# Performance work log

Measured on AMD Instinct MI355X. Metric: run time of the kernel, lower is better.

## Reference

```python
import jax, jax.numpy as jnp
import numpy as np

N_QUBITS = 8
N_LAYERS = 4
DIM = 2 ** N_QUBITS  # 256 state-vector

# PauliZ sign table: signs[i, idx] = +1 if bit of wire i in basis index idx is 0 else -1.
# Wire 0 is the most-significant axis (state axes ordered wire0..wire{n-1}).
_idx = np.arange(DIM)
SIGNS = np.stack([1.0 - 2.0 * ((_idx >> (N_QUBITS - 1 - i)) & 1) for i in range(N_QUBITS)]).astype(np.float32)  # [n, 256]


def _rx_mat(theta):
    c = jnp.cos(0.5 * theta).astype(jnp.complex64)
    s = (-1j * jnp.sin(0.5 * theta)).astype(jnp.complex64)
    return jnp.stack([jnp.stack([c, s]), jnp.stack([s, c])])  # [2,2]


def _rz_diag(theta):
    return jnp.stack([jnp.exp(-0.5j * theta), jnp.exp(0.5j * theta)]).astype(jnp.complex64)  # [2]


def _apply_1q(state, U, w):
    # state: (2,)*n complex64; apply 2x2 U on wire w
    st = jnp.moveaxis(state, w, 0).reshape(2, -1)
    st = U @ st
    return jnp.moveaxis(st.reshape((2,) * N_QUBITS), 0, w)


def _apply_diag(state, d, w):
    st = jnp.moveaxis(state, w, 0)
    st = st * d.reshape((2,) + (1,) * (N_QUBITS - 1))
    return jnp.moveaxis(st, 0, w)


def _cnot(state, c, t):
    st = jnp.moveaxis(state, (c, t), (0, 1))
    st = jnp.stack([st[0], st[1][::-1]], axis=0)  # flip target where control==1
    return jnp.moveaxis(st, (0, 1), (c, t))


def _circuit(angles, weights):
    # angles: [n_qubits], weights: [n_layers, 2, n_qubits] -> expvals [n_qubits]
    state = jnp.zeros((2,) * N_QUBITS, jnp.complex64).at[(0,) * N_QUBITS].set(1.0)
    for i in range(N_QUBITS):
        state = _apply_1q(state, _rx_mat(angles[i]), i)
        state = _apply_diag(state, _rz_diag(angles[i]), i)
    for l in range(N_LAYERS):
        for i in range(N_QUBITS):
            state = _apply_1q(state, _rx_mat(weights[l, 0, i]), i)
            state = _apply_diag(state, _rz_diag(weights[l, 1, i]), i)
        for i in range(N_QUBITS - 1):
            state = _cnot(state, i, i + 1)
    probs = jnp.abs(state.reshape(-1)) ** 2  # [256]
    return (probs @ SIGNS.T).astype(jnp.float32)  # [n_qubits] <Z_i>


def setup_inputs() -> dict:
    key = jax.random.key(0)
    B, D_IN, D_OUT = 8192, 1024, 1024
    ks = jax.random.split(key, 6)
    bound_in = np.sqrt(6.0 / D_IN)  # kaiming_uniform fan_in, linear
    bound_out = np.sqrt(6.0 / N_QUBITS)
    return {
        "x": jax.random.normal(ks[0], (B, D_IN), jnp.float32),
        "W_in": jax.random.uniform(ks[1], (N_QUBITS, D_IN), jnp.float32, -bound_in, bound_in),
        "b_in": jnp.zeros((N_QUBITS,), jnp.float32),
        "q_weights": jax.random.uniform(ks[2], (N_LAYERS, 2, N_QUBITS), jnp.float32, 0.0, 2.0 * np.pi),
        "W_out": jax.random.uniform(ks[3], (D_OUT, N_QUBITS), jnp.float32, -bound_out, bound_out),
        "b_out": jnp.zeros((D_OUT,), jnp.float32),
    }


def reference(x, W_in, b_in, q_weights, W_out, b_out):
    x_proj = x @ W_in.T + b_in                                   # [B, n_qubits]
    ev = jax.vmap(_circuit, in_axes=(0, None))(x_proj, q_weights)  # [B, n_qubits]
    return ev @ W_out.T + b_out                                   # [B, output_dim]
```

## Files before the change

### kernel.cpp

```cpp
#include <hip/hip_runtime.h>
#include <math.h>


typedef float f32x2 __attribute__((ext_vector_type(2)));

__device__ __forceinline__ int f2i(float v) { return __float_as_int(v); }
__device__ __forceinline__ float i2f(int v) { return __int_as_float(v); }

template <int CTRL>
__device__ __forceinline__ float dppf(float v) {
    return i2f(__builtin_amdgcn_update_dpp(0, f2i(v), CTRL, 0xF, 0xF, true));
}

template <int ML>
__device__ __forceinline__ float gshm(float v) {
    static_assert(ML > 0 && ML < 64, "lane mask");
    if constexpr (ML == 1)      return dppf<0xB1>(v);
    else if constexpr (ML == 2) return dppf<0x4E>(v);
    else if constexpr (ML == 3) return dppf<0x1B>(v);
    else if constexpr (ML == 8) return dppf<0x128>(v);
    else if constexpr (ML < 32) return i2f(__builtin_amdgcn_ds_swizzle(f2i(v), 0x1F | (ML << 10)));
    else                        return __shfl_xor(v, ML, 64);
}

template <int L>
__device__ __forceinline__ float rdlane(float v) {
    return i2f(__builtin_amdgcn_readlane(f2i(v), L));
}

template <int ML, int MR, int ZL, int ZR>
__device__ __forceinline__ void ggate(f32x2& reA, f32x2& reB, f32x2& imA, f32x2& imB,
                                      float c1, float s1, float c2, float s2,
                                      int lane) {
    f32x2 sReA, sReB, sImA, sImB;
    if constexpr (MR == 0)      { sReA = reA;    sReB = reB;    sImA = imA;    sImB = imB; }
    else if constexpr (MR == 1) { sReA = reA.yx; sReB = reB.yx; sImA = imA.yx; sImB = imB.yx; }
    else if constexpr (MR == 2) { sReA = reB;    sReB = reA;    sImA = imB;    sImB = imA; }
    else                        { sReA = reB.yx; sReB = reA.yx; sImA = imB.yx; sImB = imA.yx; }
    f32x2 pReA, pReB, pImA, pImB;
    if constexpr (ML != 0) {
        pReA.x = gshm<ML>(sReA.x); pReA.y = gshm<ML>(sReA.y);
        pReB.x = gshm<ML>(sReB.x); pReB.y = gshm<ML>(sReB.y);
        pImA.x = gshm<ML>(sImA.x); pImA.y = gshm<ML>(sImA.y);
        pImB.x = gshm<ML>(sImB.x); pImB.y = gshm<ML>(sImB.y);
    } else { pReA = sReA; pReB = sReB; pImA = sImA; pImB = sImB; }
    f32x2 nReA = c1 * reA + s1 * pImA;
    f32x2 nReB = c1 * reB + s1 * pImB;
    f32x2 nImA = c1 * imA - s1 * pReA;
    f32x2 nImB = c1 * imB - s1 * pReB;
    float base;
    if constexpr (ZL == 0) base = -s2;
    else                   base = (__popc(lane & ZL) & 1) ? s2 : -s2;
    constexpr bool N1 = (ZR & 1) != 0;
    constexpr bool N2 = ((ZR >> 1) & 1) != 0;
    constexpr bool N3 = (((ZR & 1) ^ ((ZR >> 1) & 1)) != 0);
    f32x2 ssA = { base, N1 ? -base : base };
    f32x2 ssB = { N2 ? -base : base, N3 ? -base : base };
    f32x2 tA = c2 * nReA - ssA * nImA;
    f32x2 tB = c2 * nReB - ssB * nImB;
    imA = c2 * nImA + ssA * nReA;
    imB = c2 * nImB + ssB * nReB;
    reA = tA;
    reB = tB;
}

__global__ void __launch_bounds__(256, 8) qasa_kernel(
    const float* __restrict__ x, const float* __restrict__ W_in,
    const float* __restrict__ b_in, const float* __restrict__ qw,
    const float* __restrict__ W_out, const float* __restrict__ b_out,
    float* __restrict__ out)
{
    const int tid = threadIdx.x;
    const int lane = tid & 63;
    const int w = tid >> 6;
    const int block4 = blockIdx.x * 4;

    __shared__ float ang[32];
    __shared__ float evs[4][8] __attribute__((aligned(16)));

    float vc, vs;
    __sincosf(0.5f * qw[lane], &vs, &vc);

    const int b0 = lane & 1, b1 = (lane >> 1) & 1, b3 = (lane >> 3) & 1;
    const int qofl = b0 | (b1 << 1) | (b3 << 2);
    const float binq = b_in[qofl];

    {
        const float4* w4 = (const float4*)W_in;
        const float4* xr0 = (const float4*)(x + (size_t)block4 * 1024);
        f32x2 acc2[8];
#pragma unroll
        for (int j = 0; j < 8; ++j) acc2[j] = (f32x2){0.f, 0.f};
#pragma unroll
        for (int k = 0; k < 4; ++k) {
            float4 wv0 = w4[(2 * w) * 256 + lane + 64 * k];
            float4 wv1 = w4[(2 * w + 1) * 256 + lane + 64 * k];
#pragma unroll
            for (int r = 0; r < 4; ++r) {
                float4 xvv = xr0[r * 256 + lane + 64 * k];
                acc2[r]     += (f32x2){xvv.x, xvv.y} * (f32x2){wv0.x, wv0.y}
                             + (f32x2){xvv.z, xvv.w} * (f32x2){wv0.z, wv0.w};
                acc2[4 + r] += (f32x2){xvv.x, xvv.y} * (f32x2){wv1.x, wv1.y}
                             + (f32x2){xvv.z, xvv.w} * (f32x2){wv1.z, wv1.w};
            }
        }
        float acc[8];
#pragma unroll
        for (int j = 0; j < 8; ++j) {
            acc[j] = acc2[j].x + acc2[j].y;
            acc[j] += dppf<0xB1>(acc[j]);
            acc[j] += dppf<0x4E>(acc[j]);
            acc[j] += dppf<0x128>(acc[j]);
        }
        float t01 = b0 ? acc[1] : acc[0];
        float t23 = b0 ? acc[3] : acc[2];
        float t45 = b0 ? acc[5] : acc[4];
        float t67 = b0 ? acc[7] : acc[6];
        float ta = b1 ? t23 : t01;
        float tb = b1 ? t67 : t45;
        float S = b3 ? tb : ta;
        S += gshm<4>(S); S += gshm<16>(S); S += gshm<32>(S);
        if ((lane & 52) == 0)
            ang[(2 * w + ((lane >> 3) & 1)) * 4 + (lane & 3)] = S;
    }
    __syncthreads();

    float A = ang[qofl * 4 + w] + binq;
    float ca, sa;
    __sincosf(0.5f * A, &sa, &ca);
    float ur = ca * ca, ui = -ca * sa, vr = sa * sa, vi = ui;
    const int a1 = 4 * qofl, a2 = 4 * (qofl + 8);
    float cx = i2f(__builtin_amdgcn_ds_bpermute(a1, f2i(vc)));
    float sx = i2f(__builtin_amdgcn_ds_bpermute(a1, f2i(vs)));
    float cz = i2f(__builtin_amdgcn_ds_bpermute(a2, f2i(vc)));
    float sz = i2f(__builtin_amdgcn_ds_bpermute(a2, f2i(vs)));
    float ur1 = cx * ur + sx * vi, ui1 = cx * ui - sx * vr;
    float vr1 = cx * vr + sx * ui, vi1 = cx * vi - sx * ur;
    float ur2 = cz * ur1 + sz * ui1, ui2 = cz * ui1 - sz * ur1;
    float vr2 = cz * vr1 - sz * vi1, vi2 = cz * vi1 + sz * vr1;

    float Pr, Pi;
    {
        float fur = rdlane<0>(ur2), fui = rdlane<0>(ui2);
        float fvr = rdlane<0>(vr2), fvi = rdlane<0>(vi2);
        bool b = (lane >> 5) & 1;
        Pr = b ? fvr : fur;
        Pi = b ? fvi : fui;
    }
#define PMUL(W_, L_) { \
        float fur = rdlane<L_>(ur2), fui = rdlane<L_>(ui2); \
        float fvr = rdlane<L_>(vr2), fvi = rdlane<L_>(vi2); \
        bool b = (lane >> (5 - (W_))) & 1; \
        float fr = b ? fvr : fur, fi = b ? fvi : fui; \
        float tr = Pr * fr - Pi * fi; \
        Pi = Pr * fi + Pi * fr; \
        Pr = tr; }
    PMUL(1, 1) PMUL(2, 2) PMUL(3, 3) PMUL(4, 8) PMUL(5, 9)
#undef PMUL
    f32x2 reA, reB, imA, imB;
    {
        float u6r = rdlane<10>(ur2), u6i = rdlane<10>(ui2);
        float v6r = rdlane<10>(vr2), v6i = rdlane<10>(vi2);
        float u7r = rdlane<11>(ur2), u7i = rdlane<11>(ui2);
        float v7r = rdlane<11>(vr2), v7i = rdlane<11>(vi2);
        float rr[4], ii[4];
#pragma unroll
        for (int r = 0; r < 4; ++r) {
            float g6r_ = (r & 2) ? v6r : u6r, g6i_ = (r & 2) ? v6i : u6i;
            float g7r_ = (r & 1) ? v7r : u7r, g7i_ = (r & 1) ? v7i : u7i;
            float fr = g6r_ * g7r_ - g6i_ * g7i_;
            float fi = g6r_ * g7i_ + g6i_ * g7r_;
            rr[r] = Pr * fr - Pi * fi;
            ii[r] = Pr * fi + Pi * fr;
        }
        reA = (f32x2){ rr[0], rr[1] };  reB = (f32x2){ rr[2], rr[3] };
        imA = (f32x2){ ii[0], ii[1] };  imB = (f32x2){ ii[2], ii[3] };
    }

#define GG(Lx, W_, ML_, MR_, ZL_, ZR_) \
    ggate<ML_, MR_, ZL_, ZR_>(reA, reB, imA, imB, \
        rdlane<16 * (Lx) + (W_)>(vc), rdlane<16 * (Lx) + (W_)>(vs), \
        rdlane<16 * (Lx) + 8 + (W_)>(vc), rdlane<16 * (Lx) + 8 + (W_)>(vs), lane);

    GG(1,0, 48,0, 32,0)  GG(1,1, 24,0, 48,0)  GG(1,2, 12,0, 56,0) GG(1,3, 6,0, 60,0)
    GG(1,4, 3,0, 62,0)   GG(1,5, 1,2, 63,0)   GG(1,6, 0,3, 63,2)  GG(1,7, 0,1, 63,3)
    GG(2,0, 40,0, 32,0)  GG(2,1, 20,0, 16,0)  GG(2,2, 10,0, 40,0) GG(2,3, 5,0, 20,0)
    GG(2,4, 2,2, 42,0)   GG(2,5, 1,1, 21,0)   GG(2,6, 0,2, 42,2)  GG(2,7, 0,1, 21,1)
    GG(3,0, 60,0, 32,0)  GG(3,1, 30,0, 48,0)  GG(3,2, 15,0, 24,0) GG(3,3, 7,2, 12,0)
    GG(3,4, 3,3, 38,0)   GG(3,5, 1,3, 51,0)   GG(3,6, 0,3, 25,2)  GG(3,7, 0,1, 12,3)
#undef GG

    {
        float p0 = reA.x * reA.x + imA.x * imA.x;
        float p1 = reA.y * reA.y + imA.y * imA.y;
        float p2 = reB.x * reB.x + imB.x * imB.x;
        float p3 = reB.y * reB.y + imB.y * imB.y;
        float q0 = (p0 + p1) + (p2 + p3);
        float q2 = (p0 + p1) - (p2 + p3);
        float q1 = (p0 + p2) - (p1 + p3);

        float v = q0;
        { float u = dppf<0xB1>(v);  v = (lane & 1)  ? (u - v) : (v + u); }
        { float u = dppf<0x4E>(v);  v = (lane & 2)  ? (u - v) : (v + u); }
        { float u = dppf<0x128>(v); v = (lane & 8)  ? (u - v) : (v + u); }
        { float u = gshm<4>(v);     v = (lane & 4)  ? (u - v) : (v + u); }
        { float u = gshm<16>(v);    v = (lane & 16) ? (u - v) : (v + u); }
        { float u = gshm<32>(v);    v = (lane & 32) ? (u - v) : (v + u); }

        q2 += dppf<0xB1>(q2);
        q2 += dppf<0x4E>(q2);
        { float u = dppf<0x128>(q2); q2 = (lane & 8) ? (u - q2) : (q2 + u); }
        q2 += gshm<4>(q2); q2 += gshm<16>(q2); q2 += gshm<32>(q2);

        q1 += dppf<0xB1>(q1);
        q1 += dppf<0x4E>(q1);
        q1 += dppf<0x128>(q1);
        { float u = gshm<4>(q1); q1 = (lane & 4) ? (u - q1) : (q1 + u); }
        q1 += gshm<16>(q1); q1 += gshm<32>(q1);

        const unsigned long long wrmask = 0x0000000500030110ULL;
        if ((wrmask >> lane) & 1) {
            int k = 6 - __ffs(lane);
            evs[w][k] = v;
        }
        if (lane == 8) { evs[w][6] = q2; }
        if (lane == 4) { evs[w][7] = q1; }
    }
    __syncthreads();

    {
        const int c4 = (w << 6) + lane;
        const float4* wo = (const float4*)W_out;
        float4 wa[4], wb[4];
#pragma unroll
        for (int c = 0; c < 4; ++c) {
            wa[c] = wo[2 * (4 * c4 + c)];
            wb[c] = wo[2 * (4 * c4 + c) + 1];
        }
        float4 bias = ((const float4*)b_out)[c4];
#pragma unroll
        for (int r = 0; r < 4; ++r) {
            const float4* ev4 = (const float4*)evs[r];
            float4 lo = ev4[0], hi = ev4[1];
            f32x2 E01 = { lo.x, lo.y }, E23 = { lo.z, lo.w };
            f32x2 E45 = { hi.x, hi.y }, E67 = { hi.z, hi.w };
            float res[4];
#pragma unroll
            for (int c = 0; c < 4; ++c) {
                f32x2 a2v = E01 * (f32x2){ wa[c].x, wa[c].y } + E23 * (f32x2){ wa[c].z, wa[c].w }
                          + E45 * (f32x2){ wb[c].x, wb[c].y } + E67 * (f32x2){ wb[c].z, wb[c].w };
                res[c] = a2v.x + a2v.y;
            }
            float4 o;
            o.x = bias.x + res[0]; o.y = bias.y + res[1];
            o.z = bias.z + res[2]; o.w = bias.w + res[3];
            ((float4*)(out + (size_t)(block4 + r) * 1024))[c4] = o;
        }
    }
}

extern "C" void kernel_launch(void* const* d_in, const int* in_sizes, int n_in,
                              void* d_out, int out_size, void* d_ws, size_t ws_size,
                              hipStream_t stream) {
    const float* x     = (const float*)d_in[0];
    const float* W_in  = (const float*)d_in[1];
    const float* b_in  = (const float*)d_in[2];
    const float* qw    = (const float*)d_in[3];
    const float* W_out = (const float*)d_in[4];
    const float* b_out = (const float*)d_in[5];
    float* outp = (float*)d_out;

    const int B = in_sizes[0] / 1024;
    const int grid = B / 4;
    qasa_kernel<<<grid, 256, 0, stream>>>(x, W_in, b_in, qw, W_out, b_out, outp);
}
```

Before: 110.1 us.

## Replace unrolled gate templates with a table-driven rolled loop using bpermute

Swaps the 24 fully unrolled, compile-time-specialized gate applications for a runtime loop driven by a packed constant table, with all lane exchanges done through ds_bpermute. Readlanes use dynamic lane indices, and the PMUL chain becomes a rolled loop. Launch bounds drop from 8 to 4 waves per SIMD. The goal is smaller code and less instruction-cache pressure, paid for with slower LDS-based permutes in place of DPP/swizzle, dynamic readlane, runtime selects and loop overhead.

```diff
diff --git a/kernel.cpp b/kernel.cpp
--- a/kernel.cpp
+++ b/kernel.cpp
@@ -27,44 +27,14 @@
 __device__ __forceinline__ float rdlane(float v) {
     return i2f(__builtin_amdgcn_readlane(f2i(v), L));
 }
-
-template <int ML, int MR, int ZL, int ZR>
-__device__ __forceinline__ void ggate(f32x2& reA, f32x2& reB, f32x2& imA, f32x2& imB,
-                                      float c1, float s1, float c2, float s2,
-                                      int lane) {
-    f32x2 sReA, sReB, sImA, sImB;
-    if constexpr (MR == 0)      { sReA = reA;    sReB = reB;    sImA = imA;    sImB = imB; }
-    else if constexpr (MR == 1) { sReA = reA.yx; sReB = reB.yx; sImA = imA.yx; sImB = imB.yx; }
-    else if constexpr (MR == 2) { sReA = reB;    sReB = reA;    sImA = imB;    sImB = imA; }
-    else                        { sReA = reB.yx; sReB = reA.yx; sImA = imB.yx; sImB = imA.yx; }
-    f32x2 pReA, pReB, pImA, pImB;
-    if constexpr (ML != 0) {
-        pReA.x = gshm<ML>(sReA.x); pReA.y = gshm<ML>(sReA.y);
-        pReB.x = gshm<ML>(sReB.x); pReB.y = gshm<ML>(sReB.y);
-        pImA.x = gshm<ML>(sImA.x); pImA.y = gshm<ML>(sImA.y);
-        pImB.x = gshm<ML>(sImB.x); pImB.y = gshm<ML>(sImB.y);
-    } else { pReA = sReA; pReB = sReB; pImA = sImA; pImB = sImB; }
-    f32x2 nReA = c1 * reA + s1 * pImA;
-    f32x2 nReB = c1 * reB + s1 * pImB;
-    f32x2 nImA = c1 * imA - s1 * pReA;
-    f32x2 nImB = c1 * imB - s1 * pReB;
-    float base;
-    if constexpr (ZL == 0) base = -s2;
-    else                   base = (__popc(lane & ZL) & 1) ? s2 : -s2;
-    constexpr bool N1 = (ZR & 1) != 0;
-    constexpr bool N2 = ((ZR >> 1) & 1) != 0;
-    constexpr bool N3 = (((ZR & 1) ^ ((ZR >> 1) & 1)) != 0);
-    f32x2 ssA = { base, N1 ? -base : base };
-    f32x2 ssB = { N2 ? -base : base, N3 ? -base : base };
-    f32x2 tA = c2 * nReA - ssA * nImA;
-    f32x2 tB = c2 * nReB - ssB * nImB;
-    imA = c2 * nImA + ssA * nReA;
-    imB = c2 * nImB + ssB * nReB;
-    reA = tA;
-    reB = tB;
-}
-
-__global__ void __launch_bounds__(256, 8) qasa_kernel(
+__device__ __forceinline__ float rdlv(float v, int l) {
+    return i2f(__builtin_amdgcn_readlane(f2i(v), l));
+}
+__device__ __forceinline__ float bperm(int addr, float v) {
+    return i2f(__builtin_amdgcn_ds_bpermute(addr, f2i(v)));
+}
+
+__global__ void __launch_bounds__(256, 4) qasa_kernel(
     const float* __restrict__ x, const float* __restrict__ W_in,
     const float* __restrict__ b_in, const float* __restrict__ qw,
     const float* __restrict__ W_out, const float* __restrict__ b_out,
@@ -130,10 +100,10 @@
     __sincosf(0.5f * A, &sa, &ca);
     float ur = ca * ca, ui = -ca * sa, vr = sa * sa, vi = ui;
     const int a1 = 4 * qofl, a2 = 4 * (qofl + 8);
-    float cx = i2f(__builtin_amdgcn_ds_bpermute(a1, f2i(vc)));
-    float sx = i2f(__builtin_amdgcn_ds_bpermute(a1, f2i(vs)));
-    float cz = i2f(__builtin_amdgcn_ds_bpermute(a2, f2i(vc)));
-    float sz = i2f(__builtin_amdgcn_ds_bpermute(a2, f2i(vs)));
+    float cx = bperm(a1, vc);
+    float sx = bperm(a1, vs);
+    float cz = bperm(a2, vc);
+    float sz = bperm(a2, vs);
     float ur1 = cx * ur + sx * vi, ui1 = cx * ui - sx * vr;
     float vr1 = cx * vr + sx * ui, vi1 = cx * vi - sx * ur;
     float ur2 = cz * ur1 + sz * ui1, ui2 = cz * ui1 - sz * ur1;
@@ -147,16 +117,17 @@
         Pr = b ? fvr : fur;
         Pi = b ? fvi : fui;
     }
-#define PMUL(W_, L_) { \
-        float fur = rdlane<L_>(ur2), fui = rdlane<L_>(ui2); \
-        float fvr = rdlane<L_>(vr2), fvi = rdlane<L_>(vi2); \
-        bool b = (lane >> (5 - (W_))) & 1; \
-        float fr = b ? fvr : fur, fi = b ? fvi : fui; \
-        float tr = Pr * fr - Pi * fi; \
-        Pi = Pr * fi + Pi * fr; \
-        Pr = tr; }
-    PMUL(1, 1) PMUL(2, 2) PMUL(3, 3) PMUL(4, 8) PMUL(5, 9)
-#undef PMUL
+#pragma unroll 1
+    for (int W = 1; W <= 5; ++W) {
+        const int fl = W + ((W >> 2) << 2);
+        float fur = rdlv(ur2, fl), fui = rdlv(ui2, fl);
+        float fvr = rdlv(vr2, fl), fvi = rdlv(vi2, fl);
+        bool b = (lane >> (5 - W)) & 1;
+        float fr = b ? fvr : fur, fi = b ? fvi : fui;
+        float tr = Pr * fr - Pi * fi;
+        Pi = Pr * fi + Pi * fr;
+        Pr = tr;
+    }
     f32x2 reA, reB, imA, imB;
     {
         float u6r = rdlane<10>(ur2), u6i = rdlane<10>(ui2);
@@ -177,18 +148,49 @@
         imA = (f32x2){ ii[0], ii[1] };  imB = (f32x2){ ii[2], ii[3] };
     }
 
-#define GG(Lx, W_, ML_, MR_, ZL_, ZR_) \
-    ggate<ML_, MR_, ZL_, ZR_>(reA, reB, imA, imB, \
-        rdlane<16 * (Lx) + (W_)>(vc), rdlane<16 * (Lx) + (W_)>(vs), \
-        rdlane<16 * (Lx) + 8 + (W_)>(vc), rdlane<16 * (Lx) + 8 + (W_)>(vs), lane);
-
-    GG(1,0, 48,0, 32,0)  GG(1,1, 24,0, 48,0)  GG(1,2, 12,0, 56,0) GG(1,3, 6,0, 60,0)
-    GG(1,4, 3,0, 62,0)   GG(1,5, 1,2, 63,0)   GG(1,6, 0,3, 63,2)  GG(1,7, 0,1, 63,3)
-    GG(2,0, 40,0, 32,0)  GG(2,1, 20,0, 16,0)  GG(2,2, 10,0, 40,0) GG(2,3, 5,0, 20,0)
-    GG(2,4, 2,2, 42,0)   GG(2,5, 1,1, 21,0)   GG(2,6, 0,2, 42,2)  GG(2,7, 0,1, 21,1)
-    GG(3,0, 60,0, 32,0)  GG(3,1, 30,0, 48,0)  GG(3,2, 15,0, 24,0) GG(3,3, 7,2, 12,0)
-    GG(3,4, 3,3, 38,0)   GG(3,5, 1,3, 51,0)   GG(3,6, 0,3, 25,2)  GG(3,7, 0,1, 12,3)
-#undef GG
+    static const unsigned TB[24] = {
+        0x00200030u, 0x00300018u, 0x0038000Cu, 0x003C0006u,
+        0x003E0003u, 0x003F0201u, 0x023F0300u, 0x033F0100u,
+        0x00200028u, 0x00100014u, 0x0028000Au, 0x00140005u,
+        0x002A0202u, 0x00150101u, 0x022A0200u, 0x01150100u,
+        0x0020003Cu, 0x0030001Eu, 0x0018000Fu, 0x000C0207u,
+        0x00260303u, 0x00330301u, 0x02190300u, 0x030C0100u,
+    };
+#pragma unroll 1
+    for (int g = 0; g < 24; ++g) {
+        const unsigned tb = TB[g];
+        const int ML = tb & 255;
+        const int MR = (tb >> 8) & 255;
+        const int ZL = (tb >> 16) & 255;
+        const int ZR = (int)(tb >> 24);
+        const int lx = 16 * (1 + (g >> 3)) + (g & 7);
+        const float c1 = rdlv(vc, lx),     s1 = rdlv(vs, lx);
+        const float c2 = rdlv(vc, lx + 8), s2 = rdlv(vs, lx + 8);
+        const bool jm = (MR & 2) != 0, cm = (MR & 1) != 0;
+        f32x2 sReA = jm ? reB : reA, sReB = jm ? reA : reB;
+        f32x2 sImA = jm ? imB : imA, sImB = jm ? imA : imB;
+        if (cm) { sReA = sReA.yx; sReB = sReB.yx; sImA = sImA.yx; sImB = sImB.yx; }
+        const int pa = (lane ^ ML) << 2;
+        f32x2 pReA, pReB, pImA, pImB;
+        pReA.x = bperm(pa, sReA.x); pReA.y = bperm(pa, sReA.y);
+        pReB.x = bperm(pa, sReB.x); pReB.y = bperm(pa, sReB.y);
+        pImA.x = bperm(pa, sImA.x); pImA.y = bperm(pa, sImA.y);
+        pImB.x = bperm(pa, sImB.x); pImB.y = bperm(pa, sImB.y);
+        f32x2 nReA = c1 * reA + s1 * pImA;
+        f32x2 nReB = c1 * reB + s1 * pImB;
+        f32x2 nImA = c1 * imA - s1 * pReA;
+        f32x2 nImB = c1 * imB - s1 * pReB;
+        const float base = (__popc(lane & ZL) & 1) ? s2 : -s2;
+        const bool n1 = (ZR & 1) != 0, n2 = (ZR & 2) != 0;
+        f32x2 ssA = { base,              n1 ? -base : base };
+        f32x2 ssB = { n2 ? -base : base, (n1 != n2) ? -base : base };
+        f32x2 tA = c2 * nReA - ssA * nImA;
+        f32x2 tB = c2 * nReB - ssB * nImB;
+        imA = c2 * nImA + ssA * nReA;
+        imB = c2 * nImB + ssB * nReB;
+        reA = tA;
+        reB = tB;
+    }
 
     {
         float p0 = reA.x * reA.x + imA.x * imA.x;
```

Result: slower. 115.8 us (+5.2%).
